# Kernel optimization log

Measured on AMD Instinct MI355X. Metric: run time of the kernel, lower is better.

Reference implementation:

```python
import jax, jax.numpy as jnp
import numpy as np

N_TOKENS = 2048
HIDDEN = 2048
N_EXPERTS = 8
TOP_K = 2
D_FF = 1408  # per-expert SwiGLU intermediate size


def setup_inputs() -> dict:
    key = jax.random.key(0)
    k_h, k_g, k_wg, k_wu, k_wd = jax.random.split(key, 5)
    s_in = 1.0 / np.sqrt(HIDDEN)
    s_ff = 1.0 / np.sqrt(D_FF)
    return {
        "h": jax.random.normal(k_h, (N_TOKENS, HIDDEN), dtype=jnp.float32),
        "gate_w": jax.random.normal(k_g, (N_EXPERTS, HIDDEN), dtype=jnp.float32) * s_in,
        "w_gate": jax.random.normal(k_wg, (N_EXPERTS, HIDDEN, D_FF), dtype=jnp.float32) * s_in,
        "w_up": jax.random.normal(k_wu, (N_EXPERTS, HIDDEN, D_FF), dtype=jnp.float32) * s_in,
        "w_down": jax.random.normal(k_wd, (N_EXPERTS, D_FF, HIDDEN), dtype=jnp.float32) * s_ff,
    }


def reference(h, gate_w, w_gate, w_up, w_down):
    # --- gate: linear (fp32) + softmax + top-k (no renorm, as in source) ---
    logits = jnp.einsum("nd,ed->ne", h.astype(jnp.float32), gate_w.astype(jnp.float32))
    scores = jax.nn.softmax(logits, axis=-1)                 # [N, E]
    topk_weight, topk_idx = jax.lax.top_k(scores, TOP_K)     # [N, K], [N, K]

    # --- per-expert SwiGLU MLP applied densely, then gather selected experts ---
    # (same math as the per-expert grouped GEMM dispatch in the eager loop)
    g = jnp.einsum("nd,edf->enf", h, w_gate)                 # [E, N, F]
    u = jnp.einsum("nd,edf->enf", h, w_up)                   # [E, N, F]
    y = jnp.einsum("enf,efd->end", jax.nn.silu(g) * u, w_down)  # [E, N, D]

    # gather each token's top-k expert outputs: [N, K, D]
    y_tok = jnp.transpose(y, (1, 0, 2))                      # [N, E, D]
    sel = jnp.take_along_axis(y_tok, topk_idx[:, :, None], axis=1)

    # weighted combine
    out = jnp.einsum("nk,nkd->nd", topk_weight.astype(h.dtype), sel)
    return out
```

## Files before the change

### kernel.cpp

```cpp
#include <hip/hip_runtime.h>
#include <hip/hip_bf16.h>
#include <stdint.h>

#define N_TOK 2048
#define HID   2048
#define NEXP  8
#define DFF   1408

typedef __attribute__((ext_vector_type(8))) short short8;
typedef __attribute__((ext_vector_type(4))) float f32x4;

__device__ __forceinline__ unsigned short f2bf(float f) {
  union { float ff; uint32_t u; } v; v.ff = f;
  return (unsigned short)((v.u + 0x7FFFu + ((v.u >> 16) & 1u)) >> 16);
}
__device__ __forceinline__ float bf2f(unsigned short u) {
  union { uint32_t i; float f; } v; v.i = (uint32_t)u << 16; return v.f;
}

__device__ __forceinline__ void gl2lds16(const void* g, void* l) {
  __builtin_amdgcn_global_load_lds(
      (const __attribute__((address_space(1))) void*)g,
      (__attribute__((address_space(3))) void*)l, 16, 0, 0);
}

#define MFMA16(a, b, c) __builtin_amdgcn_mfma_f32_16x16x32_bf16((a), (b), (c), 0, 0, 0)

__global__ __launch_bounds__(256) void gate_topk_k(
    const float* __restrict__ h, const float* __restrict__ gw,
    int* __restrict__ cnt, int* __restrict__ topk_idx, float* __restrict__ topk_w,
    unsigned short* __restrict__ hbf)
{
  int token = blockIdx.x * 4 + (threadIdx.x >> 6);
  int lane  = threadIdx.x & 63;
  const float* hr = h + (size_t)token * HID;
  float acc[NEXP];
#pragma unroll
  for (int e = 0; e < NEXP; ++e) acc[e] = 0.f;
  for (int c = lane * 8; c < HID; c += 512) {
    float4 a = *(const float4*)(hr + c);
    float4 b = *(const float4*)(hr + c + 4);
    unsigned short o[8] = {f2bf(a.x), f2bf(a.y), f2bf(a.z), f2bf(a.w),
                           f2bf(b.x), f2bf(b.y), f2bf(b.z), f2bf(b.w)};
    *(short8*)&hbf[(size_t)token * HID + c] = *(const short8*)o;
#pragma unroll
    for (int e = 0; e < NEXP; ++e) {
      const float* gp = gw + (size_t)e * HID + c;
      float4 ga = *(const float4*)gp;
      float4 gb = *(const float4*)(gp + 4);
      acc[e] = fmaf(a.x, ga.x, fmaf(a.y, ga.y, fmaf(a.z, ga.z, fmaf(a.w, ga.w,
               fmaf(b.x, gb.x, fmaf(b.y, gb.y, fmaf(b.z, gb.z, fmaf(b.w, gb.w, acc[e]))))))));
    }
  }
#pragma unroll
  for (int e = 0; e < NEXP; ++e) {
    float a = acc[e];
#pragma unroll
    for (int s = 32; s > 0; s >>= 1) a += __shfl_xor(a, s, 64);
    acc[e] = a;
  }
  if (lane == 0) {
    float m = acc[0];
#pragma unroll
    for (int e = 1; e < NEXP; ++e) m = fmaxf(m, acc[e]);
    float w[NEXP]; float s = 0.f;
#pragma unroll
    for (int e = 0; e < NEXP; ++e) { w[e] = __expf(acc[e] - m); s += w[e]; }
    float inv = 1.f / s;
    int i0 = 0; float b0 = acc[0];
#pragma unroll
    for (int e = 1; e < NEXP; ++e) if (acc[e] > b0) { b0 = acc[e]; i0 = e; }
    int i1 = -1; float b1 = -3.4e38f;
#pragma unroll
    for (int e = 0; e < NEXP; ++e) if (e != i0 && acc[e] > b1) { b1 = acc[e]; i1 = e; }
    topk_idx[token * 2 + 0] = i0;
    topk_idx[token * 2 + 1] = i1;
    topk_w[token * 2 + 0] = w[i0] * inv;
    topk_w[token * 2 + 1] = w[i1] * inv;
    atomicAdd(&cnt[i0], 1);
    atomicAdd(&cnt[i1], 1);
  }
}

__global__ void prefix_k(const int* __restrict__ cnt, int* __restrict__ offs,
                         int* __restrict__ cursor) {
  if (threadIdx.x == 0 && blockIdx.x == 0) {
    int s = 0;
    for (int e = 0; e < NEXP; ++e) { offs[e] = s; cursor[e] = s; s += cnt[e]; }
  }
}

__global__ __launch_bounds__(256) void scatter_k(
    const int* __restrict__ topk_idx, const float* __restrict__ topk_w,
    int* __restrict__ cursor, int* __restrict__ pair_token, float* __restrict__ pair_w,
    int* __restrict__ tok_slot)
{
  int n = blockIdx.x * 256 + threadIdx.x;
  if (n >= N_TOK) return;
#pragma unroll
  for (int k = 0; k < 2; ++k) {
    int e = topk_idx[n * 2 + k];
    int p = atomicAdd(&cursor[e], 1);
    pair_token[p] = n;
    pair_w[p] = topk_w[n * 2 + k];
    tok_slot[n * 2 + k] = p;
  }
}

__global__ __launch_bounds__(256) void transpose_k(const float* __restrict__ s1,
                                                   unsigned short* __restrict__ d1,
                                                   const float* __restrict__ s2,
                                                   unsigned short* __restrict__ d2,
                                                   int R, int C, int nz1)
{
  __shared__ unsigned short T[64 * 66];
  const size_t sl = (size_t)R * C;
  int z = blockIdx.z;
  const float* s; unsigned short* d;
  if (z < nz1) { s = s1 + (size_t)z * sl; d = d1 + (size_t)z * sl; }
  else { s = s2 + (size_t)(z - nz1) * sl; d = d2 + (size_t)(z - nz1) * sl; }
  const int rb = blockIdx.x * 64, cb = blockIdx.y * 64;
  const int t = threadIdx.x;
  const int tr = t >> 4, tc = (t & 15) * 4;
  const float* sp = s + (size_t)(rb + tr) * C + cb + tc;
#pragma unroll
  for (int i = 0; i < 4; ++i) {
    float4 v = *(const float4*)(sp + (size_t)i * 16 * C);
    int r = tr + i * 16;
    uint32_t p0 = (uint32_t)f2bf(v.x) | ((uint32_t)f2bf(v.y) << 16);
    uint32_t p1 = (uint32_t)f2bf(v.z) | ((uint32_t)f2bf(v.w) << 16);
    *(uint32_t*)&T[r * 66 + tc]     = p0;
    *(uint32_t*)&T[r * 66 + tc + 2] = p1;
  }
  __syncthreads();
  const int f = t >> 2, ch = (t & 3) * 16;
  unsigned short* dp = d + (size_t)(cb + f) * R + rb + ch;
#pragma unroll
  for (int g = 0; g < 2; ++g) {
    unsigned short buf[8];
#pragma unroll
    for (int j = 0; j < 8; ++j) buf[j] = T[(ch + g * 8 + j) * 66 + f];
    *(short8*)(dp + g * 8) = *(const short8*)buf;
  }
}

__global__ __launch_bounds__(256) void gateup11_k(
    const unsigned short* __restrict__ hbf,
    const unsigned short* __restrict__ wgt, const unsigned short* __restrict__ wut,
    const int* __restrict__ cnt, const int* __restrict__ offs,
    const int* __restrict__ pair_token, unsigned short* __restrict__ act,
    int e_fixed, int nw, int nbcnt, size_t wstride)
{
  const int x = blockIdx.x;
  const int wti = x % nw, mb = x / nw;
  int e, nb;
  if (e_fixed >= 0) { e = e_fixed; nb = wti; }
  else { e = wti / nbcnt; nb = wti % nbcnt; }
  const int count = cnt[e];
  if (mb * 64 >= count) return;
  const int off = offs[e];
  const int rows = min(64, count - mb * 64);
  const int c0 = nb * 64;

  __shared__ unsigned short As[3][64 * 64];
  __shared__ unsigned short Bg[3][64 * 64];
  __shared__ unsigned short Bu[3][64 * 64];
  __shared__ int tok[64];

  const int t = threadIdx.x;
  if (t < 64) tok[t] = pair_token[off + mb * 64 + min(t, rows - 1)];
  __syncthreads();

  const int w = t >> 6, l = t & 63;
  const int sr = l >> 3;
  const int sc = ((l & 7) ^ sr) * 8;
  const int r0 = w * 16 + sr, r1 = w * 16 + 8 + sr;

  const size_t wb = (e_fixed >= 0) ? 0 : (size_t)e * wstride;
  const unsigned short* wgE = wgt + wb;
  const unsigned short* wuE = wut + wb;
  const unsigned short* aP0 = hbf + (size_t)tok[r0] * HID + sc;
  const unsigned short* aP1 = hbf + (size_t)tok[r1] * HID + sc;
  const unsigned short* gP0 = wgE + (size_t)(c0 + r0) * HID + sc;
  const unsigned short* gP1 = wgE + (size_t)(c0 + r1) * HID + sc;
  const unsigned short* uP0 = wuE + (size_t)(c0 + r0) * HID + sc;
  const unsigned short* uP1 = wuE + (size_t)(c0 + r1) * HID + sc;
  const int ldsLo = (w * 16) * 64, ldsHi = (w * 16 + 8) * 64;

  const int fr = l & 15, fq = l >> 4;
  const int wr = (w >> 1) * 32, wc = (w & 1) * 32;
  const int f3 = fr & 7;

  f32x4 accg[2][2], accu[2][2];
#pragma unroll
  for (int i = 0; i < 2; ++i)
#pragma unroll
    for (int j = 0; j < 2; ++j) {
      accg[i][j] = (f32x4){0.f, 0.f, 0.f, 0.f};
      accu[i][j] = (f32x4){0.f, 0.f, 0.f, 0.f};
    }

  auto stage = [&](int b, int kt) {
    gl2lds16(aP0 + kt, &As[b][ldsLo]); gl2lds16(aP1 + kt, &As[b][ldsHi]);
    gl2lds16(gP0 + kt, &Bg[b][ldsLo]); gl2lds16(gP1 + kt, &Bg[b][ldsHi]);
    gl2lds16(uP0 + kt, &Bu[b][ldsLo]); gl2lds16(uP1 + kt, &Bu[b][ldsHi]);
  };
  auto compute = [&](int b) {
    short8 af[2][2], bg[2][2], bu[2][2];
#pragma unroll
    for (int kk = 0; kk < 2; ++kk) {
      const int ch = ((kk * 4 + fq) ^ f3) * 8;
#pragma unroll
      for (int mi = 0; mi < 2; ++mi)
        af[mi][kk] = *(const short8*)&As[b][(wr + mi * 16 + fr) * 64 + ch];
#pragma unroll
      for (int ni = 0; ni < 2; ++ni) {
        bg[ni][kk] = *(const short8*)&Bg[b][(wc + ni * 16 + fr) * 64 + ch];
        bu[ni][kk] = *(const short8*)&Bu[b][(wc + ni * 16 + fr) * 64 + ch];
      }
    }
    __builtin_amdgcn_s_setprio(1);
#pragma unroll
    for (int kk = 0; kk < 2; ++kk)
#pragma unroll
      for (int mi = 0; mi < 2; ++mi)
#pragma unroll
        for (int ni = 0; ni < 2; ++ni) {
          accg[mi][ni] = MFMA16(af[mi][kk], bg[ni][kk], accg[mi][ni]);
          accu[mi][ni] = MFMA16(af[mi][kk], bu[ni][kk], accu[mi][ni]);
        }
    __builtin_amdgcn_s_setprio(0);
  };

  const int NK = HID / 64;
  stage(0, 0);
  int cur = 0;
  for (int k = 0; k < NK; ++k) {
    if (k + 1 < NK) {
      int bn = cur + 1; if (bn >= 3) bn -= 3;
      stage(bn, (k + 1) * 64);
      asm volatile("s_waitcnt vmcnt(6)" ::: "memory");
    } else {
      asm volatile("s_waitcnt vmcnt(0)" ::: "memory");
    }
    asm volatile("s_barrier" ::: "memory");
    compute(cur);
    cur = (cur + 1 < 3) ? cur + 1 : 0;
  }

#pragma unroll
  for (int mi = 0; mi < 2; ++mi)
#pragma unroll
    for (int ni = 0; ni < 2; ++ni)
#pragma unroll
      for (int j = 0; j < 4; ++j) {
        int r = wr + mi * 16 + fq * 4 + j;
        if (r < rows) {
          float g = accg[mi][ni][j], u = accu[mi][ni][j];
          float a = (g / (1.f + __expf(-g))) * u;
          act[(size_t)(off + mb * 64 + r) * DFF + (c0 + wc + ni * 16 + fr)] = f2bf(a);
        }
      }
}

__global__ __launch_bounds__(256) void down11_k(
    const unsigned short* __restrict__ act, const unsigned short* __restrict__ wdt,
    const int* __restrict__ cnt, const int* __restrict__ offs,
    unsigned short* __restrict__ ypair, int e_fixed, int nw, int nbcnt, size_t wstride)
{
  const int x = blockIdx.x;
  const int wti = x % nw, mb = x / nw;
  int e, nb;
  if (e_fixed >= 0) { e = e_fixed; nb = wti; }
  else { e = wti / nbcnt; nb = wti % nbcnt; }
  const int count = cnt[e];
  if (mb * 64 >= count) return;
  const int off = offs[e];
  const int rows = min(64, count - mb * 64);
  const int c0 = nb * 128;

  __shared__ unsigned short As[3][64 * 64];
  __shared__ unsigned short Bd[3][128 * 64];

  const int t = threadIdx.x;
  const int w = t >> 6, l = t & 63;
  const int sr = l >> 3;
  const int sc = ((l & 7) ^ sr) * 8;
  const size_t wb = (e_fixed >= 0) ? 0 : (size_t)e * wstride;
  const unsigned short* wdE = wdt + wb;

  const int ra0 = min(w * 16 + sr, rows - 1), ra1 = min(w * 16 + 8 + sr, rows - 1);
  const unsigned short* aP0 = act + (size_t)(off + mb * 64 + ra0) * DFF + sc;
  const unsigned short* aP1 = act + (size_t)(off + mb * 64 + ra1) * DFF + sc;
  const int ldsALo = (w * 16) * 64, ldsAHi = (w * 16 + 8) * 64;
  const unsigned short* bP[4];
  int ldsB[4];
#pragma unroll
  for (int i = 0; i < 4; ++i) {
    int rr = w * 32 + i * 8 + sr;
    bP[i] = wdE + (size_t)(c0 + rr) * DFF + sc;
    ldsB[i] = (w * 32 + i * 8) * 64;
  }

  const int fr = l & 15, fq = l >> 4;
  const int wr = (w >> 1) * 32, wc = (w & 1) * 64;
  const int f3 = fr & 7;

  f32x4 acc[2][4];
#pragma unroll
  for (int i = 0; i < 2; ++i)
#pragma unroll
    for (int j = 0; j < 4; ++j) acc[i][j] = (f32x4){0.f, 0.f, 0.f, 0.f};

  auto stage = [&](int b, int kt) {
    gl2lds16(aP0 + kt, &As[b][ldsALo]);
    gl2lds16(aP1 + kt, &As[b][ldsAHi]);
#pragma unroll
    for (int i = 0; i < 4; ++i) gl2lds16(bP[i] + kt, &Bd[b][ldsB[i]]);
  };
  auto compute = [&](int b) {
    short8 af[2][2], bd[4][2];
#pragma unroll
    for (int kk = 0; kk < 2; ++kk) {
      const int ch = ((kk * 4 + fq) ^ f3) * 8;
#pragma unroll
      for (int mi = 0; mi < 2; ++mi)
        af[mi][kk] = *(const short8*)&As[b][(wr + mi * 16 + fr) * 64 + ch];
#pragma unroll
      for (int ni = 0; ni < 4; ++ni)
        bd[ni][kk] = *(const short8*)&Bd[b][(wc + ni * 16 + fr) * 64 + ch];
    }
    __builtin_amdgcn_s_setprio(1);
#pragma unroll
    for (int kk = 0; kk < 2; ++kk)
#pragma unroll
      for (int mi = 0; mi < 2; ++mi)
#pragma unroll
        for (int ni = 0; ni < 4; ++ni)
          acc[mi][ni] = MFMA16(af[mi][kk], bd[ni][kk], acc[mi][ni]);
    __builtin_amdgcn_s_setprio(0);
  };

  const int NK = DFF / 64;
  stage(0, 0);
  int cur = 0;
  for (int k = 0; k < NK; ++k) {
    if (k + 1 < NK) {
      int bn = cur + 1; if (bn >= 3) bn -= 3;
      stage(bn, (k + 1) * 64);
      asm volatile("s_waitcnt vmcnt(6)" ::: "memory");
    } else {
      asm volatile("s_waitcnt vmcnt(0)" ::: "memory");
    }
    asm volatile("s_barrier" ::: "memory");
    compute(cur);
    cur = (cur + 1 < 3) ? cur + 1 : 0;
  }

#pragma unroll
  for (int mi = 0; mi < 2; ++mi)
#pragma unroll
    for (int ni = 0; ni < 4; ++ni)
#pragma unroll
      for (int j = 0; j < 4; ++j) {
        int r = wr + mi * 16 + fq * 4 + j;
        if (r < rows)
          ypair[(size_t)(off + mb * 64 + r) * HID + (c0 + wc + ni * 16 + fr)] = f2bf(acc[mi][ni][j]);
      }
}

__global__ __launch_bounds__(256) void combine_k(
    const unsigned short* __restrict__ ypair, const int* __restrict__ tok_slot,
    const float* __restrict__ topk_w, float* __restrict__ out)
{
  int i = blockIdx.x * 256 + threadIdx.x;
  int n = i >> 8;
  int dv = (i & 255) * 8;
  int s0 = tok_slot[n * 2], s1 = tok_slot[n * 2 + 1];
  float w0 = topk_w[n * 2], w1 = topk_w[n * 2 + 1];
  short8 a = *(const short8*)&ypair[(size_t)s0 * HID + dv];
  short8 b = *(const short8*)&ypair[(size_t)s1 * HID + dv];
  float o[8];
#pragma unroll
  for (int j = 0; j < 8; ++j)
    o[j] = w0 * bf2f((unsigned short)a[j]) + w1 * bf2f((unsigned short)b[j]);
  *(float4*)&out[(size_t)n * HID + dv]     = *(const float4*)&o[0];
  *(float4*)&out[(size_t)n * HID + dv + 4] = *(const float4*)&o[4];
}

extern "C" void kernel_launch(void* const* d_in, const int* in_sizes, int n_in,
                              void* d_out, int out_size, void* d_ws, size_t ws_size,
                              hipStream_t stream) {
  const float* h  = (const float*)d_in[0];
  const float* gw = (const float*)d_in[1];
  const float* wg = (const float*)d_in[2];
  const float* wu = (const float*)d_in[3];
  const float* wd = (const float*)d_in[4];
  float* out = (float*)d_out;

  const size_t SL = (size_t)DFF * HID;
  char* ws = (char*)d_ws;
  int*   cnt        = (int*)(ws + 0);
  int*   offs       = (int*)(ws + 32);
  int*   cursor     = (int*)(ws + 64);
  int*   pair_token = (int*)(ws + 256);
  float* pair_w     = (float*)(ws + 16640);
  int*   tok_slot   = (int*)(ws + 33024);
  int*   topk_idx   = (int*)(ws + 49408);
  float* topk_w     = (float*)(ws + 65792);
  unsigned short* act = (unsigned short*)(ws + 82176);
  unsigned short* hbf = (unsigned short*)(ws + 11616512);
  unsigned short* wgt = (unsigned short*)(ws + 20005120);
  unsigned short* wut = (unsigned short*)(ws + 66142464);
  unsigned short* ypair_full = (unsigned short*)(ws + 66142464);
  const size_t NEED_FULL = 112279808ull;

  hipMemsetAsync(ws, 0, 256, stream);

  gate_topk_k<<<N_TOK / 4, 256, 0, stream>>>(h, gw, cnt, topk_idx, topk_w, hbf);
  prefix_k<<<1, 64, 0, stream>>>(cnt, offs, cursor);
  scatter_k<<<N_TOK / 256, 256, 0, stream>>>(topk_idx, topk_w, cursor, pair_token, pair_w, tok_slot);

  if (ws_size >= NEED_FULL) {
    transpose_k<<<dim3(HID / 64, DFF / 64, 16), 256, 0, stream>>>(wg, wgt, wu, wut, HID, DFF, 8);
    gateup11_k<<<176 * 16, 256, 0, stream>>>(hbf, wgt, wut, cnt, offs, pair_token, act,
                                             -1, 176, 22, SL);
    transpose_k<<<dim3(DFF / 64, HID / 64, 8), 256, 0, stream>>>(wd, wgt, wd, wgt, DFF, HID, 8);
    down11_k<<<128 * 16, 256, 0, stream>>>(act, wgt, cnt, offs, ypair_full,
                                           -1, 128, 16, SL);
    combine_k<<<(N_TOK * HID / 8) / 256, 256, 0, stream>>>(ypair_full, tok_slot, topk_w, out);
  } else {
    unsigned short* wgtE = (unsigned short*)(ws + 20005120);
    unsigned short* wutE = (unsigned short*)(ws + 25772288);
    unsigned short* ypair = (unsigned short*)(ws + 31539456);
    for (int e = 0; e < NEXP; ++e) {
      transpose_k<<<dim3(HID / 64, DFF / 64, 2), 256, 0, stream>>>(wg + e * SL, wgtE, wu + e * SL, wutE, HID, DFF, 1);
      gateup11_k<<<22 * 16, 256, 0, stream>>>(hbf, wgtE, wutE, cnt, offs, pair_token, act,
                                              e, 22, 22, 0);
    }
    for (int e = 0; e < NEXP; ++e) {
      transpose_k<<<dim3(DFF / 64, HID / 64, 1), 256, 0, stream>>>(wd + e * SL, wgtE, wd + e * SL, wgtE, DFF, HID, 1);
      down11_k<<<16 * 16, 256, 0, stream>>>(act, wgtE, cnt, offs, ypair, e, 16, 16, 0);
    }
    combine_k<<<(N_TOK * HID / 8) / 256, 256, 0, stream>>>(ypair, tok_slot, topk_w, out);
  }
}
```

Before: 322.5 us.

## Restructure MoE GEMMs to 128-row tiles with persistent M loop, single-buffered K=32

Rewrites the gate/up and down expert GEMM kernels to use 128-row M tiles with K steps of 32, and has each block loop over M tiles with stride 8 instead of launching one block per 64-row tile. This halves the grid and doubles per-block output reuse of the weight tiles. In exchange it drops the triple-buffered async pipeline and setprio scheduling for a single LDS buffer with two barriers per K step, so global-load latency is no longer overlapped with MFMA work. It also doubles the number of K iterations.

```diff
diff --git a/kernel.cpp b/kernel.cpp
--- a/kernel.cpp
+++ b/kernel.cpp
@@ -144,7 +144,7 @@
   }
 }
 
-__global__ __launch_bounds__(256) void gateup11_k(
+__global__ __launch_bounds__(256) void gateup12_k(
     const unsigned short* __restrict__ hbf,
     const unsigned short* __restrict__ wgt, const unsigned short* __restrict__ wut,
     const int* __restrict__ cnt, const int* __restrict__ offs,
@@ -152,221 +152,176 @@
     int e_fixed, int nw, int nbcnt, size_t wstride)
 {
   const int x = blockIdx.x;
-  const int wti = x % nw, mb = x / nw;
+  const int wti = x % nw;
   int e, nb;
   if (e_fixed >= 0) { e = e_fixed; nb = wti; }
   else { e = wti / nbcnt; nb = wti % nbcnt; }
   const int count = cnt[e];
-  if (mb * 64 >= count) return;
   const int off = offs[e];
-  const int rows = min(64, count - mb * 64);
   const int c0 = nb * 64;
 
-  __shared__ unsigned short As[3][64 * 64];
-  __shared__ unsigned short Bg[3][64 * 64];
-  __shared__ unsigned short Bu[3][64 * 64];
-  __shared__ int tok[64];
+  __shared__ unsigned short As[128 * 32];
+  __shared__ unsigned short Bg[64 * 32];
+  __shared__ unsigned short Bu[64 * 32];
+  __shared__ int tok[128];
 
   const int t = threadIdx.x;
-  if (t < 64) tok[t] = pair_token[off + mb * 64 + min(t, rows - 1)];
-  __syncthreads();
-
   const int w = t >> 6, l = t & 63;
-  const int sr = l >> 3;
-  const int sc = ((l & 7) ^ sr) * 8;
-  const int r0 = w * 16 + sr, r1 = w * 16 + 8 + sr;
+  const int lr = l >> 2;
+  const int lp = l & 3;
+  const int sc = (lp ^ (lr & 3)) * 8;
 
   const size_t wb = (e_fixed >= 0) ? 0 : (size_t)e * wstride;
-  const unsigned short* wgE = wgt + wb;
-  const unsigned short* wuE = wut + wb;
-  const unsigned short* aP0 = hbf + (size_t)tok[r0] * HID + sc;
-  const unsigned short* aP1 = hbf + (size_t)tok[r1] * HID + sc;
-  const unsigned short* gP0 = wgE + (size_t)(c0 + r0) * HID + sc;
-  const unsigned short* gP1 = wgE + (size_t)(c0 + r1) * HID + sc;
-  const unsigned short* uP0 = wuE + (size_t)(c0 + r0) * HID + sc;
-  const unsigned short* uP1 = wuE + (size_t)(c0 + r1) * HID + sc;
-  const int ldsLo = (w * 16) * 64, ldsHi = (w * 16 + 8) * 64;
+  const unsigned short* gP = wgt + wb + (size_t)(c0 + w * 16 + lr) * HID + sc;
+  const unsigned short* uP = wut + wb + (size_t)(c0 + w * 16 + lr) * HID + sc;
 
   const int fr = l & 15, fq = l >> 4;
-  const int wr = (w >> 1) * 32, wc = (w & 1) * 32;
-  const int f3 = fr & 7;
-
-  f32x4 accg[2][2], accu[2][2];
-#pragma unroll
-  for (int i = 0; i < 2; ++i)
-#pragma unroll
-    for (int j = 0; j < 2; ++j) {
-      accg[i][j] = (f32x4){0.f, 0.f, 0.f, 0.f};
-      accu[i][j] = (f32x4){0.f, 0.f, 0.f, 0.f};
+  const int wr = (w >> 1) * 64, wc = (w & 1) * 32;
+
+  for (int mb = x / nw; mb * 128 < count; mb += 8) {
+    const int m0 = mb * 128;
+    const int rows = min(128, count - m0);
+    if (t < 128) tok[t] = pair_token[off + m0 + min(t, rows - 1)];
+    __syncthreads();
+
+    const unsigned short* aP0 = hbf + (size_t)tok[w * 32 + lr] * HID + sc;
+    const unsigned short* aP1 = hbf + (size_t)tok[w * 32 + 16 + lr] * HID + sc;
+
+    f32x4 accg[4][2], accu[4][2];
+#pragma unroll
+    for (int i = 0; i < 4; ++i)
+#pragma unroll
+      for (int j = 0; j < 2; ++j) {
+        accg[i][j] = (f32x4){0.f, 0.f, 0.f, 0.f};
+        accu[i][j] = (f32x4){0.f, 0.f, 0.f, 0.f};
+      }
+
+    for (int kt = 0; kt < HID; kt += 32) {
+      gl2lds16(aP0 + kt, &As[(w * 32) * 32]);
+      gl2lds16(aP1 + kt, &As[(w * 32 + 16) * 32]);
+      gl2lds16(gP + kt, &Bg[(w * 16) * 32]);
+      gl2lds16(uP + kt, &Bu[(w * 16) * 32]);
+      __syncthreads();
+
+      short8 af[4], bg[2], bu[2];
+#pragma unroll
+      for (int mi = 0; mi < 4; ++mi) {
+        int r = wr + mi * 16 + fr;
+        af[mi] = *(const short8*)&As[r * 32 + ((fq ^ (r & 3)) * 8)];
+      }
+#pragma unroll
+      for (int ni = 0; ni < 2; ++ni) {
+        int rb = wc + ni * 16 + fr;
+        bg[ni] = *(const short8*)&Bg[rb * 32 + ((fq ^ (rb & 3)) * 8)];
+        bu[ni] = *(const short8*)&Bu[rb * 32 + ((fq ^ (rb & 3)) * 8)];
+      }
+#pragma unroll
+      for (int mi = 0; mi < 4; ++mi)
+#pragma unroll
+        for (int ni = 0; ni < 2; ++ni) {
+          accg[mi][ni] = MFMA16(af[mi], bg[ni], accg[mi][ni]);
+          accu[mi][ni] = MFMA16(af[mi], bu[ni], accu[mi][ni]);
+        }
+      __syncthreads();
     }
 
-  auto stage = [&](int b, int kt) {
-    gl2lds16(aP0 + kt, &As[b][ldsLo]); gl2lds16(aP1 + kt, &As[b][ldsHi]);
-    gl2lds16(gP0 + kt, &Bg[b][ldsLo]); gl2lds16(gP1 + kt, &Bg[b][ldsHi]);
-    gl2lds16(uP0 + kt, &Bu[b][ldsLo]); gl2lds16(uP1 + kt, &Bu[b][ldsHi]);
-  };
-  auto compute = [&](int b) {
-    short8 af[2][2], bg[2][2], bu[2][2];
-#pragma unroll
-    for (int kk = 0; kk < 2; ++kk) {
-      const int ch = ((kk * 4 + fq) ^ f3) * 8;
-#pragma unroll
-      for (int mi = 0; mi < 2; ++mi)
-        af[mi][kk] = *(const short8*)&As[b][(wr + mi * 16 + fr) * 64 + ch];
-#pragma unroll
-      for (int ni = 0; ni < 2; ++ni) {
-        bg[ni][kk] = *(const short8*)&Bg[b][(wc + ni * 16 + fr) * 64 + ch];
-        bu[ni][kk] = *(const short8*)&Bu[b][(wc + ni * 16 + fr) * 64 + ch];
-      }
-    }
-    __builtin_amdgcn_s_setprio(1);
-#pragma unroll
-    for (int kk = 0; kk < 2; ++kk)
-#pragma unroll
-      for (int mi = 0; mi < 2; ++mi)
-#pragma unroll
-        for (int ni = 0; ni < 2; ++ni) {
-          accg[mi][ni] = MFMA16(af[mi][kk], bg[ni][kk], accg[mi][ni]);
-          accu[mi][ni] = MFMA16(af[mi][kk], bu[ni][kk], accu[mi][ni]);
+#pragma unroll
+    for (int mi = 0; mi < 4; ++mi)
+#pragma unroll
+      for (int ni = 0; ni < 2; ++ni)
+#pragma unroll
+        for (int j = 0; j < 4; ++j) {
+          int r = wr + mi * 16 + fq * 4 + j;
+          if (r < rows) {
+            float g = accg[mi][ni][j], u = accu[mi][ni][j];
+            float a = (g / (1.f + __expf(-g))) * u;
+            act[(size_t)(off + m0 + r) * DFF + (c0 + wc + ni * 16 + fr)] = f2bf(a);
+          }
         }
-    __builtin_amdgcn_s_setprio(0);
-  };
-
-  const int NK = HID / 64;
-  stage(0, 0);
-  int cur = 0;
-  for (int k = 0; k < NK; ++k) {
-    if (k + 1 < NK) {
-      int bn = cur + 1; if (bn >= 3) bn -= 3;
-      stage(bn, (k + 1) * 64);
-      asm volatile("s_waitcnt vmcnt(6)" ::: "memory");
-    } else {
-      asm volatile("s_waitcnt vmcnt(0)" ::: "memory");
-    }
-    asm volatile("s_barrier" ::: "memory");
-    compute(cur);
-    cur = (cur + 1 < 3) ? cur + 1 : 0;
-  }
-
-#pragma unroll
-  for (int mi = 0; mi < 2; ++mi)
-#pragma unroll
-    for (int ni = 0; ni < 2; ++ni)
-#pragma unroll
-      for (int j = 0; j < 4; ++j) {
-        int r = wr + mi * 16 + fq * 4 + j;
-        if (r < rows) {
-          float g = accg[mi][ni][j], u = accu[mi][ni][j];
-          float a = (g / (1.f + __expf(-g))) * u;
-          act[(size_t)(off + mb * 64 + r) * DFF + (c0 + wc + ni * 16 + fr)] = f2bf(a);
-        }
-      }
-}
-
-__global__ __launch_bounds__(256) void down11_k(
+  }
+}
+
+__global__ __launch_bounds__(256) void down12_k(
     const unsigned short* __restrict__ act, const unsigned short* __restrict__ wdt,
     const int* __restrict__ cnt, const int* __restrict__ offs,
     unsigned short* __restrict__ ypair, int e_fixed, int nw, int nbcnt, size_t wstride)
 {
   const int x = blockIdx.x;
-  const int wti = x % nw, mb = x / nw;
+  const int wti = x % nw;
   int e, nb;
   if (e_fixed >= 0) { e = e_fixed; nb = wti; }
   else { e = wti / nbcnt; nb = wti % nbcnt; }
   const int count = cnt[e];
-  if (mb * 64 >= count) return;
   const int off = offs[e];
-  const int rows = min(64, count - mb * 64);
   const int c0 = nb * 128;
 
-  __shared__ unsigned short As[3][64 * 64];
-  __shared__ unsigned short Bd[3][128 * 64];
+  __shared__ unsigned short As[128 * 32];
+  __shared__ unsigned short Bd[128 * 32];
 
   const int t = threadIdx.x;
   const int w = t >> 6, l = t & 63;
-  const int sr = l >> 3;
-  const int sc = ((l & 7) ^ sr) * 8;
+  const int lr = l >> 2;
+  const int lp = l & 3;
+  const int sc = (lp ^ (lr & 3)) * 8;
+
   const size_t wb = (e_fixed >= 0) ? 0 : (size_t)e * wstride;
-  const unsigned short* wdE = wdt + wb;
-
-  const int ra0 = min(w * 16 + sr, rows - 1), ra1 = min(w * 16 + 8 + sr, rows - 1);
-  const unsigned short* aP0 = act + (size_t)(off + mb * 64 + ra0) * DFF + sc;
-  const unsigned short* aP1 = act + (size_t)(off + mb * 64 + ra1) * DFF + sc;
-  const int ldsALo = (w * 16) * 64, ldsAHi = (w * 16 + 8) * 64;
-  const unsigned short* bP[4];
-  int ldsB[4];
-#pragma unroll
-  for (int i = 0; i < 4; ++i) {
-    int rr = w * 32 + i * 8 + sr;
-    bP[i] = wdE + (size_t)(c0 + rr) * DFF + sc;
-    ldsB[i] = (w * 32 + i * 8) * 64;
-  }
+  const unsigned short* bP0 = wdt + wb + (size_t)(c0 + w * 32 + lr) * DFF + sc;
+  const unsigned short* bP1 = wdt + wb + (size_t)(c0 + w * 32 + 16 + lr) * DFF + sc;
 
   const int fr = l & 15, fq = l >> 4;
-  const int wr = (w >> 1) * 32, wc = (w & 1) * 64;
-  const int f3 = fr & 7;
-
-  f32x4 acc[2][4];
-#pragma unroll
-  for (int i = 0; i < 2; ++i)
-#pragma unroll
-    for (int j = 0; j < 4; ++j) acc[i][j] = (f32x4){0.f, 0.f, 0.f, 0.f};
-
-  auto stage = [&](int b, int kt) {
-    gl2lds16(aP0 + kt, &As[b][ldsALo]);
-    gl2lds16(aP1 + kt, &As[b][ldsAHi]);
-#pragma unroll
-    for (int i = 0; i < 4; ++i) gl2lds16(bP[i] + kt, &Bd[b][ldsB[i]]);
-  };
-  auto compute = [&](int b) {
-    short8 af[2][2], bd[4][2];
-#pragma unroll
-    for (int kk = 0; kk < 2; ++kk) {
-      const int ch = ((kk * 4 + fq) ^ f3) * 8;
-#pragma unroll
-      for (int mi = 0; mi < 2; ++mi)
-        af[mi][kk] = *(const short8*)&As[b][(wr + mi * 16 + fr) * 64 + ch];
+  const int wr = (w >> 1) * 64, wc = (w & 1) * 64;
+
+  for (int mb = x / nw; mb * 128 < count; mb += 8) {
+    const int m0 = mb * 128;
+    const int rows = min(128, count - m0);
+    const int ra0 = min(w * 32 + lr, rows - 1);
+    const int ra1 = min(w * 32 + 16 + lr, rows - 1);
+    const unsigned short* aP0 = act + (size_t)(off + m0 + ra0) * DFF + sc;
+    const unsigned short* aP1 = act + (size_t)(off + m0 + ra1) * DFF + sc;
+
+    f32x4 acc[4][4];
+#pragma unroll
+    for (int i = 0; i < 4; ++i)
+#pragma unroll
+      for (int j = 0; j < 4; ++j) acc[i][j] = (f32x4){0.f, 0.f, 0.f, 0.f};
+
+    for (int kt = 0; kt < DFF; kt += 32) {
+      gl2lds16(aP0 + kt, &As[(w * 32) * 32]);
+      gl2lds16(aP1 + kt, &As[(w * 32 + 16) * 32]);
+      gl2lds16(bP0 + kt, &Bd[(w * 32) * 32]);
+      gl2lds16(bP1 + kt, &Bd[(w * 32 + 16) * 32]);
+      __syncthreads();
+
+      short8 af[4], bd[4];
+#pragma unroll
+      for (int mi = 0; mi < 4; ++mi) {
+        int r = wr + mi * 16 + fr;
+        af[mi] = *(const short8*)&As[r * 32 + ((fq ^ (r & 3)) * 8)];
+      }
+#pragma unroll
+      for (int ni = 0; ni < 4; ++ni) {
+        int rb = wc + ni * 16 + fr;
+        bd[ni] = *(const short8*)&Bd[rb * 32 + ((fq ^ (rb & 3)) * 8)];
+      }
+#pragma unroll
+      for (int mi = 0; mi < 4; ++mi)
+#pragma unroll
+        for (int ni = 0; ni < 4; ++ni)
+          acc[mi][ni] = MFMA16(af[mi], bd[ni], acc[mi][ni]);
+      __syncthreads();
+    }
+
+#pragma unroll
+    for (int mi = 0; mi < 4; ++mi)
 #pragma unroll
       for (int ni = 0; ni < 4; ++ni)
-        bd[ni][kk] = *(const short8*)&Bd[b][(wc + ni * 16 + fr) * 64 + ch];
-    }
-    __builtin_amdgcn_s_setprio(1);
-#pragma unroll
-    for (int kk = 0; kk < 2; ++kk)
-#pragma unroll
-      for (int mi = 0; mi < 2; ++mi)
-#pragma unroll
-        for (int ni = 0; ni < 4; ++ni)
-          acc[mi][ni] = MFMA16(af[mi][kk], bd[ni][kk], acc[mi][ni]);
-    __builtin_amdgcn_s_setprio(0);
-  };
-
-  const int NK = DFF / 64;
-  stage(0, 0);
-  int cur = 0;
-  for (int k = 0; k < NK; ++k) {
-    if (k + 1 < NK) {
-      int bn = cur + 1; if (bn >= 3) bn -= 3;
-      stage(bn, (k + 1) * 64);
-      asm volatile("s_waitcnt vmcnt(6)" ::: "memory");
-    } else {
-      asm volatile("s_waitcnt vmcnt(0)" ::: "memory");
-    }
-    asm volatile("s_barrier" ::: "memory");
-    compute(cur);
-    cur = (cur + 1 < 3) ? cur + 1 : 0;
-  }
-
-#pragma unroll
-  for (int mi = 0; mi < 2; ++mi)
-#pragma unroll
-    for (int ni = 0; ni < 4; ++ni)
-#pragma unroll
-      for (int j = 0; j < 4; ++j) {
-        int r = wr + mi * 16 + fq * 4 + j;
-        if (r < rows)
-          ypair[(size_t)(off + mb * 64 + r) * HID + (c0 + wc + ni * 16 + fr)] = f2bf(acc[mi][ni][j]);
-      }
+#pragma unroll
+        for (int j = 0; j < 4; ++j) {
+          int r = wr + mi * 16 + fq * 4 + j;
+          if (r < rows)
+            ypair[(size_t)(off + m0 + r) * HID + (c0 + wc + ni * 16 + fr)] = f2bf(acc[mi][ni][j]);
+        }
+  }
 }
 
 __global__ __launch_bounds__(256) void combine_k(
@@ -423,11 +378,11 @@
 
   if (ws_size >= NEED_FULL) {
     transpose_k<<<dim3(HID / 64, DFF / 64, 16), 256, 0, stream>>>(wg, wgt, wu, wut, HID, DFF, 8);
-    gateup11_k<<<176 * 16, 256, 0, stream>>>(hbf, wgt, wut, cnt, offs, pair_token, act,
-                                             -1, 176, 22, SL);
+    gateup12_k<<<176 * 8, 256, 0, stream>>>(hbf, wgt, wut, cnt, offs, pair_token, act,
+                                            -1, 176, 22, SL);
     transpose_k<<<dim3(DFF / 64, HID / 64, 8), 256, 0, stream>>>(wd, wgt, wd, wgt, DFF, HID, 8);
-    down11_k<<<128 * 16, 256, 0, stream>>>(act, wgt, cnt, offs, ypair_full,
-                                           -1, 128, 16, SL);
+    down12_k<<<128 * 8, 256, 0, stream>>>(act, wgt, cnt, offs, ypair_full,
+                                          -1, 128, 16, SL);
     combine_k<<<(N_TOK * HID / 8) / 256, 256, 0, stream>>>(ypair_full, tok_slot, topk_w, out);
   } else {
     unsigned short* wgtE = (unsigned short*)(ws + 20005120);
@@ -435,12 +390,12 @@
     unsigned short* ypair = (unsigned short*)(ws + 31539456);
     for (int e = 0; e < NEXP; ++e) {
       transpose_k<<<dim3(HID / 64, DFF / 64, 2), 256, 0, stream>>>(wg + e * SL, wgtE, wu + e * SL, wutE, HID, DFF, 1);
-      gateup11_k<<<22 * 16, 256, 0, stream>>>(hbf, wgtE, wutE, cnt, offs, pair_token, act,
-                                              e, 22, 22, 0);
+      gateup12_k<<<22 * 8, 256, 0, stream>>>(hbf, wgtE, wutE, cnt, offs, pair_token, act,
+                                             e, 22, 22, 0);
     }
     for (int e = 0; e < NEXP; ++e) {
       transpose_k<<<dim3(DFF / 64, HID / 64, 1), 256, 0, stream>>>(wd + e * SL, wgtE, wd + e * SL, wgtE, DFF, HID, 1);
-      down11_k<<<16 * 16, 256, 0, stream>>>(act, wgtE, cnt, offs, ypair, e, 16, 16, 0);
+      down12_k<<<16 * 8, 256, 0, stream>>>(act, wgtE, cnt, offs, ypair, e, 16, 16, 0);
     }
     combine_k<<<(N_TOK * HID / 8) / 256, 256, 0, stream>>>(ypair, tok_slot, topk_w, out);
   }
```

New measurement: 332.7 us. 3.2% more time.
